# Kernel tuning notes

Hardware: AMD Instinct MI355X
Metric: run time of the kernel (lower is better)

Reference implementation:

```python
import jax, jax.numpy as jnp
import numpy as np

N = 100000
E = 1600000
IN_C, HID, OUT_C = 3, 64, 1


def setup_inputs() -> dict:
    key = jax.random.key(0)
    ks = jax.random.split(key, 12)
    x = jax.random.normal(ks[0], (N, IN_C), dtype=jnp.float32)
    edge_index = jax.random.randint(ks[1], (2, E), 0, N, dtype=jnp.int64)

    def glorot(k, shape):
        lim = np.sqrt(6.0 / (shape[0] + shape[1]))
        return jax.random.uniform(k, shape, jnp.float32, -lim, lim)

    return {
        "x": x,
        "edge_index": edge_index,
        "W1": glorot(ks[2], (IN_C, HID)), "b1": jnp.zeros((HID,), jnp.float32),
        "W2": glorot(ks[3], (HID, HID)), "b2": jnp.zeros((HID,), jnp.float32),
        "W3": glorot(ks[4], (HID, HID)), "b3": jnp.zeros((HID,), jnp.float32),
        "Wm1": glorot(ks[5], (HID, HID)), "bm1": jnp.zeros((HID,), jnp.float32),
        "Wm2": glorot(ks[6], (HID, OUT_C)), "bm2": jnp.zeros((OUT_C,), jnp.float32),
    }


def gcn_conv(x, src, dst, W, b):
    """PyG GCNConv: symmetric normalization with self-loops, linear, scatter-add, bias."""
    n = x.shape[0]
    loop = jnp.arange(n, dtype=src.dtype)
    s = jnp.concatenate([src, loop])
    d = jnp.concatenate([dst, loop])
    h = x @ W  # (N, out)
    deg = jax.ops.segment_sum(jnp.ones(s.shape[0], dtype=h.dtype), d, num_segments=n)
    dinv = jnp.where(deg > 0, 1.0 / jnp.sqrt(jnp.where(deg > 0, deg, 1.0)), 0.0)
    norm = dinv[s] * dinv[d]  # (E+N,)
    out = jax.ops.segment_sum(h[s] * norm[:, None], d, num_segments=n)
    return out + b


def reference(x, edge_index, W1, b1, W2, b2, W3, b3, Wm1, bm1, Wm2, bm2):
    src, dst = edge_index[0], edge_index[1]
    # 3 GCN layers with ReLU (dropout inactive in eval mode)
    h = jax.nn.relu(gcn_conv(x, src, dst, W1, b1))
    h = jax.nn.relu(gcn_conv(h, src, dst, W2, b2))
    h = jax.nn.relu(gcn_conv(h, src, dst, W3, b3))
    # MLP head + sigmoid
    h = jax.nn.relu(h @ Wm1 + bm1)
    out = jax.nn.sigmoid(h @ Wm2 + bm2)  # (N, 1)
    return out
```

## Files before the change

kernel.cpp:

```cpp
#include <hip/hip_runtime.h>
#include <hip/hip_fp16.h>
#include <math.h>

#define N_NODES 100000
#define N_EDGES 1600000
#define EP (N_EDGES + N_NODES)
#define HID 64
#define NCHUNK 250
#define CE (N_EDGES / NCHUNK)
#define NBUCK 782
#define CAP 2816
#define NTILE (N_NODES / 16)
#define STASH CAP
#define OBSTRIDE 512
#define NPN 4

typedef _Float16 half8_t __attribute__((ext_vector_type(8)));
typedef _Float16 half4_t __attribute__((ext_vector_type(4)));
typedef float f32x4_t __attribute__((ext_vector_type(4)));
typedef unsigned long long u64;



__global__ void init_kernel(int* __restrict__ gcur, int* __restrict__ csr) {
    int t = threadIdx.x;
    for (int b = t; b < NBUCK; b += 512) gcur[b] = b * CAP;
    if (t < 64) csr[EP + t] = 0;
}


__global__ __launch_bounds__(1024)
void scatter_kernel(const int* __restrict__ src, const int* __restrict__ dst,
                    int* __restrict__ gcur, unsigned* __restrict__ ebuf) {
    __shared__ int hist[NBUCK];
    __shared__ int cur[NBUCK];
    const int tid = threadIdx.x, c = blockIdx.x;
    for (int b = tid; b < NBUCK; b += 1024) hist[b] = 0;
    __syncthreads();
    const int4* d4p = (const int4*)(dst + c * CE);
    const int4* s4p = (const int4*)(src + c * CE);
    for (int t = tid; t < CE / 4; t += 1024) {
        int4 d = d4p[t];
        atomicAdd(&hist[d.x >> 7], 1);
        atomicAdd(&hist[d.y >> 7], 1);
        atomicAdd(&hist[d.z >> 7], 1);
        atomicAdd(&hist[d.w >> 7], 1);
    }
    __syncthreads();
    for (int b = tid; b < NBUCK; b += 1024)
        cur[b] = hist[b] ? atomicAdd(&gcur[b], hist[b]) : 0;
    __syncthreads();
    for (int t = tid; t < CE / 4; t += 1024) {
        int4 s = s4p[t];
        int4 d = d4p[t];
        int p0 = atomicAdd(&cur[d.x >> 7], 1);
        ebuf[p0] = ((unsigned)(d.x & 127) << 17) | (unsigned)s.x;
        int p1 = atomicAdd(&cur[d.y >> 7], 1);
        ebuf[p1] = ((unsigned)(d.y & 127) << 17) | (unsigned)s.y;
        int p2 = atomicAdd(&cur[d.z >> 7], 1);
        ebuf[p2] = ((unsigned)(d.z & 127) << 17) | (unsigned)s.z;
        int p3 = atomicAdd(&cur[d.w >> 7], 1);
        ebuf[p3] = ((unsigned)(d.w & 127) << 17) | (unsigned)s.w;
    }
}


__global__ void bscan_kernel(const int* __restrict__ gcur, int* __restrict__ bR0) {
    __shared__ int tmp[1024];
    int t = threadIdx.x;
    int v = (t < NBUCK) ? (gcur[t] - t * CAP + 128) : 0;
    tmp[t] = v;
    __syncthreads();
    for (int off = 1; off < 1024; off <<= 1) {
        int y = (t >= off) ? tmp[t - off] : 0;
        __syncthreads();
        tmp[t] += y;
        __syncthreads();
    }
    if (t < NBUCK) bR0[t] = tmp[t] - v;
}


__global__ __launch_bounds__(256)
void rankfill_kernel(const unsigned* __restrict__ ebuf, const int* __restrict__ gcur,
                     const int* __restrict__ bR0, u64* __restrict__ obuf,
                     int* __restrict__ rowptr, int* __restrict__ csr,
                     float* __restrict__ dinv,
                     const float* __restrict__ x, float4* __restrict__ xd) {
    __shared__ int cnt[128];
    __shared__ int rpl[128];
    __shared__ int wsum[2];
    __shared__ int ocnt;
    __shared__ unsigned stash[STASH];
    const int tid = threadIdx.x, b = blockIdx.x;
    if (tid < 128) cnt[tid] = 0;
    if (tid == 0) ocnt = 0;
    __syncthreads();
    const int E0 = b * CAP;
    const int RL = gcur[b] - E0;
    const int R0 = bR0[b];
    for (int off = tid; off < RL; off += 256) {
        unsigned v = ebuf[E0 + off];
        int key = (v >> 17) & 0x7F;
        int r = atomicAdd(&cnt[key], 1);
        if (r < 128) {
            stash[off] = ((unsigned)r << 24) | v;
        } else {
            stash[off] = 0xFFFFFFFFu;
            int oi = atomicAdd(&ocnt, 1);
            obuf[(size_t)b * OBSTRIDE + oi] =
                ((u64)r << 40) | ((u64)key << 32) | (u64)(v & 0x1FFFFu);
        }
    }
    __syncthreads();
    const int lane = tid & 63, w = tid >> 6;
    int xcnt = (tid < 128) ? cnt[tid] : 0;
    int inc = xcnt;
#pragma unroll
    for (int off = 1; off < 64; off <<= 1) {
        int y = __shfl_up(inc, off, 64);
        if (lane >= off) inc += y;
    }
    if (lane == 63 && w < 2) wsum[w] = inc;
    __syncthreads();
    if (tid < 128) {
        int base = (w == 1) ? wsum[0] : 0;
        int pre = base + inc - xcnt;
        const int n = b * 128 + tid;
        const int rpn = R0 + tid + pre;
        rpl[tid] = rpn;
        if (n < N_NODES) {
            rowptr[n] = rpn;
            float di = rsqrtf((float)(xcnt + 1));
            dinv[n] = di;
            csr[rpn + xcnt] = n;
            xd[n] = make_float4(x[n * 3 + 0] * di, x[n * 3 + 1] * di, x[n * 3 + 2] * di, 0.f);
        }
    }
    if (b == NBUCK - 1 && tid == 0) rowptr[N_NODES] = EP;
    __syncthreads();
    for (int off = tid; off < RL; off += 256) {
        unsigned v = stash[off];
        if (v == 0xFFFFFFFFu) continue;
        csr[rpl[(v >> 17) & 0x7F] + (v >> 24)] = (int)(v & 0x1FFFFu);
    }
    for (int j = tid; j < ocnt; j += 256) {
        u64 pk = obuf[(size_t)b * OBSTRIDE + j];
        csr[rpl[(pk >> 32) & 0xFF] + (int)(pk >> 40)] = (int)(pk & 0x1FFFFu);
    }
}


__device__ __forceinline__ void addp(float4& a, uint2 u, bool pred) {
    __half2 h0 = *(__half2*)&u.x, h1 = *(__half2*)&u.y;
    float2 x = __half22float2(h0), y = __half22float2(h1);
    if (pred) { a.x += x.x; a.y += x.y; a.z += y.x; a.w += y.y; }
}

__device__ __forceinline__ void bfly_store_lds(float4 acc, const float4 b4, float di,
                                               int g, int p, int l, _Float16* __restrict__ tl) {
    acc.x += __shfl_xor(acc.x, 16, 64);
    acc.y += __shfl_xor(acc.y, 16, 64);
    acc.z += __shfl_xor(acc.z, 16, 64);
    acc.w += __shfl_xor(acc.w, 16, 64);
    acc.x += __shfl_xor(acc.x, 32, 64);
    acc.y += __shfl_xor(acc.y, 32, 64);
    acc.z += __shfl_xor(acc.z, 32, 64);
    acc.w += __shfl_xor(acc.w, 32, 64);
    if (g == 0) {
        half4_t hv;
        hv[0] = (_Float16)fmaxf(fmaf(di, acc.x, b4.x), 0.f);
        hv[1] = (_Float16)fmaxf(fmaf(di, acc.y, b4.y), 0.f);
        hv[2] = (_Float16)fmaxf(fmaf(di, acc.z, b4.z), 0.f);
        hv[3] = (_Float16)fmaxf(fmaf(di, acc.w, b4.w), 0.f);
        *(half4_t*)(tl + l * 72 + p * 4) = hv;
    }
}

__device__ __forceinline__ void gather_phase(const __half* __restrict__ gf,
                                             const int* __restrict__ rowptr,
                                             const int* __restrict__ csr,
                                             const float* __restrict__ dinv,
                                             const float* __restrict__ bias,
                                             int n0, int lane, int wid,
                                             _Float16* __restrict__ tl) {
    const int g = lane >> 4, p = lane & 15;
    const int nw = n0 + wid * NPN;
    int rp = rowptr[nw + min(lane, NPN)];
    const uint2* gf2 = (const uint2*)gf;
    const float4 b4 = ((const float4*)bias)[p];
    int begv[NPN], cntv[NPN], idxv[NPN];
    int end_prev = __shfl(rp, 0, 64);
#pragma unroll
    for (int i = 0; i < NPN; ++i) {
        int end = __shfl(rp, i + 1, 64);
        begv[i] = end_prev;
        cntv[i] = end - end_prev;
        end_prev = end;
        idxv[i] = (lane < cntv[i]) ? csr[begv[i] + lane] : 0;
    }
#pragma unroll
    for (int ii = 0; ii < NPN; ii += 2) {
        const int la = wid * NPN + ii, lb = la + 1;
        const int ca = cntv[ii], cb = cntv[ii + 1];
        const int ba = begv[ii], bb = begv[ii + 1];
        const int iva = idxv[ii], ivb = idxv[ii + 1];
        int sa0 = __shfl(iva, g, 64),      sb0 = __shfl(ivb, g, 64);
        int sa1 = __shfl(iva, g + 4, 64),  sb1 = __shfl(ivb, g + 4, 64);
        int sa2 = __shfl(iva, g + 8, 64),  sb2 = __shfl(ivb, g + 8, 64);
        int sa3 = __shfl(iva, g + 12, 64), sb3 = __shfl(ivb, g + 12, 64);
        uint2 ua0 = gf2[(size_t)sa0 * 16 + p], ub0 = gf2[(size_t)sb0 * 16 + p];
        uint2 ua1 = gf2[(size_t)sa1 * 16 + p], ub1 = gf2[(size_t)sb1 * 16 + p];
        uint2 ua2 = gf2[(size_t)sa2 * 16 + p], ub2 = gf2[(size_t)sb2 * 16 + p];
        uint2 ua3 = gf2[(size_t)sa3 * 16 + p], ub3 = gf2[(size_t)sb3 * 16 + p];
        float4 accA = make_float4(0.f, 0.f, 0.f, 0.f);
        float4 accB = make_float4(0.f, 0.f, 0.f, 0.f);
        addp(accA, ua0, g + 0 < ca);  addp(accB, ub0, g + 0 < cb);
        addp(accA, ua1, g + 4 < ca);  addp(accB, ub1, g + 4 < cb);
        addp(accA, ua2, g + 8 < ca);  addp(accB, ub2, g + 8 < cb);
        addp(accA, ua3, g + 12 < ca); addp(accB, ub3, g + 12 < cb);
        if (ca > 16) {
#pragma unroll
            for (int k = 4; k < 8; ++k) {
                int e = g + 4 * k;
                int s = __shfl(iva, e, 64);
                addp(accA, gf2[(size_t)s * 16 + p], e < ca);
            }
            if (ca > 32) {
                for (int e = 32 + g; e < ca; e += 4) {
                    int s = (e < 64) ? __shfl(iva, e, 64) : csr[ba + e];
                    addp(accA, gf2[(size_t)s * 16 + p], true);
                }
            }
        }
        if (cb > 16) {
#pragma unroll
            for (int k = 4; k < 8; ++k) {
                int e = g + 4 * k;
                int s = __shfl(ivb, e, 64);
                addp(accB, gf2[(size_t)s * 16 + p], e < cb);
            }
            if (cb > 32) {
                for (int e = 32 + g; e < cb; e += 4) {
                    int s = (e < 64) ? __shfl(ivb, e, 64) : csr[bb + e];
                    addp(accB, gf2[(size_t)s * 16 + p], true);
                }
            }
        }
        bfly_store_lds(accA, b4, dinv[n0 + la], g, p, la, tl);
        bfly_store_lds(accB, b4, dinv[n0 + lb], g, p, lb, tl);
    }
}


__global__ __launch_bounds__(256, 8)
void fused_layer1_kernel(const float4* __restrict__ xd, const int* __restrict__ rowptr,
                         const int* __restrict__ csr, const float* __restrict__ dinv,
                         const float* __restrict__ b1, const float* __restrict__ W1,
                         const float* __restrict__ W2, __half* __restrict__ gf_out) {
    __shared__ __align__(16) _Float16 tile[16 * 72];
    __shared__ __align__(16) _Float16 tile2[16 * 72];
    const int tid = threadIdx.x;
    const int lane = tid & 63, wid = tid >> 6;
    const int n0 = blockIdx.x * 16;

    const int j = lane >> 4, p = lane & 15;
    const int l = wid * 4 + j;
    const int node = n0 + l;
    const int beg = rowptr[node], end = rowptr[node + 1];
    float a0 = 0.f, a1 = 0.f, a2 = 0.f;
    for (int e = beg + p; e < end; e += 16) {
        float4 v = xd[csr[e]];
        a0 += v.x; a1 += v.y; a2 += v.z;
    }
#pragma unroll
    for (int off = 1; off < 16; off <<= 1) {
        a0 += __shfl_xor(a0, off, 64);
        a1 += __shfl_xor(a1, off, 64);
        a2 += __shfl_xor(a2, off, 64);
    }
    const float dd = dinv[node];
    const float4 w0 = ((const float4*)W1)[p];
    const float4 w1 = ((const float4*)(W1 + HID))[p];
    const float4 w2 = ((const float4*)(W1 + 2 * HID))[p];
    const float4 bb = ((const float4*)b1)[p];
    half4_t hv;
    hv[0] = (_Float16)fmaxf(fmaf(dd, a0 * w0.x + a1 * w1.x + a2 * w2.x, bb.x), 0.f);
    hv[1] = (_Float16)fmaxf(fmaf(dd, a0 * w0.y + a1 * w1.y + a2 * w2.y, bb.y), 0.f);
    hv[2] = (_Float16)fmaxf(fmaf(dd, a0 * w0.z + a1 * w1.z + a2 * w2.z, bb.z), 0.f);
    hv[3] = (_Float16)fmaxf(fmaf(dd, a0 * w0.w + a1 * w1.w + a2 * w2.w, bb.w), 0.f);
    *(half4_t*)(tile + l * 72 + p * 4) = hv;
    __syncthreads();

    const int kg = lane >> 4, n = lane & 15;
    half8_t B0, B1;
#pragma unroll
    for (int jj = 0; jj < 8; ++jj) {
        B0[jj] = (_Float16)W2[(kg * 8 + jj) * HID + wid * 16 + n];
        B1[jj] = (_Float16)W2[(32 + kg * 8 + jj) * HID + wid * 16 + n];
    }
    half8_t A0 = *(const half8_t*)(tile + n * 72 + kg * 8);
    half8_t A1 = *(const half8_t*)(tile + n * 72 + 32 + kg * 8);
    f32x4_t c = {0.f, 0.f, 0.f, 0.f};
    c = __builtin_amdgcn_mfma_f32_16x16x32_f16(A0, B0, c, 0, 0, 0);
    c = __builtin_amdgcn_mfma_f32_16x16x32_f16(A1, B1, c, 0, 0, 0);

    const int q = lane >> 4;
#pragma unroll
    for (int r = 0; r < 4; ++r)
        tile2[(q * 4 + r) * 72 + wid * 16 + n] = (_Float16)(c[r] * dinv[n0 + q * 4 + r]);
    __syncthreads();
    const int row = tid >> 4, seg = tid & 15;
    uint2 v = *(const uint2*)(tile2 + row * 72 + seg * 4);
    *(uint2*)((__half*)gf_out + (size_t)(n0 + row) * HID + seg * 4) = v;
}

__global__ __launch_bounds__(256, 8)
void fused_layer_kernel(const __half* __restrict__ gf_in, const int* __restrict__ rowptr,
                        const int* __restrict__ csr, const float* __restrict__ dinv,
                        const float* __restrict__ bias, const float* __restrict__ W,
                        __half* __restrict__ gf_out) {
    __shared__ __align__(16) _Float16 tile[16 * 72];
    __shared__ __align__(16) _Float16 tile2[16 * 72];
    const int tid = threadIdx.x;
    const int lane = tid & 63, wid = tid >> 6;
    const int n0 = blockIdx.x * 16;

    gather_phase(gf_in, rowptr, csr, dinv, bias, n0, lane, wid, tile);
    __syncthreads();

    const int kg = lane >> 4, n = lane & 15;
    half8_t B0, B1;
#pragma unroll
    for (int j = 0; j < 8; ++j) {
        B0[j] = (_Float16)W[(kg * 8 + j) * HID + wid * 16 + n];
        B1[j] = (_Float16)W[(32 + kg * 8 + j) * HID + wid * 16 + n];
    }
    half8_t A0 = *(const half8_t*)(tile + n * 72 + kg * 8);
    half8_t A1 = *(const half8_t*)(tile + n * 72 + 32 + kg * 8);
    f32x4_t c = {0.f, 0.f, 0.f, 0.f};
    c = __builtin_amdgcn_mfma_f32_16x16x32_f16(A0, B0, c, 0, 0, 0);
    c = __builtin_amdgcn_mfma_f32_16x16x32_f16(A1, B1, c, 0, 0, 0);

    const int q = lane >> 4;
#pragma unroll
    for (int r = 0; r < 4; ++r)
        tile2[(q * 4 + r) * 72 + wid * 16 + n] = (_Float16)(c[r] * dinv[n0 + q * 4 + r]);
    __syncthreads();
    const int row = tid >> 4, seg = tid & 15;
    uint2 v = *(const uint2*)(tile2 + row * 72 + seg * 4);
    *(uint2*)((__half*)gf_out + (size_t)(n0 + row) * HID + seg * 4) = v;
}


__global__ __launch_bounds__(256, 8)
void fused_final_kernel(const __half* __restrict__ gf_in, const int* __restrict__ rowptr,
                        const int* __restrict__ csr, const float* __restrict__ dinv,
                        const float* __restrict__ b3, const float* __restrict__ Wm1,
                        const float* __restrict__ bm1, const float* __restrict__ Wm2,
                        const float* __restrict__ bm2, float* __restrict__ out) {
    __shared__ __align__(16) _Float16 tile[16 * 72];
    __shared__ float redbuf[4][16];
    const int tid = threadIdx.x;
    const int lane = tid & 63, wid = tid >> 6;
    const int n0 = blockIdx.x * 16;

    gather_phase(gf_in, rowptr, csr, dinv, b3, n0, lane, wid, tile);
    __syncthreads();

    const int kg = lane >> 4, n = lane & 15;
    half8_t B0, B1;
#pragma unroll
    for (int j = 0; j < 8; ++j) {
        B0[j] = (_Float16)Wm1[(kg * 8 + j) * HID + wid * 16 + n];
        B1[j] = (_Float16)Wm1[(32 + kg * 8 + j) * HID + wid * 16 + n];
    }
    half8_t A0 = *(const half8_t*)(tile + n * 72 + kg * 8);
    half8_t A1 = *(const half8_t*)(tile + n * 72 + 32 + kg * 8);
    f32x4_t c = {0.f, 0.f, 0.f, 0.f};
    c = __builtin_amdgcn_mfma_f32_16x16x32_f16(A0, B0, c, 0, 0, 0);
    c = __builtin_amdgcn_mfma_f32_16x16x32_f16(A1, B1, c, 0, 0, 0);

    const float bm1c = bm1[wid * 16 + n];
    const float wm2c = Wm2[wid * 16 + n];
    float part[4];
#pragma unroll
    for (int r = 0; r < 4; ++r) part[r] = fmaxf(c[r] + bm1c, 0.0f) * wm2c;
#pragma unroll
    for (int off = 1; off < 16; off <<= 1)
#pragma unroll
        for (int r = 0; r < 4; ++r) part[r] += __shfl_xor(part[r], off, 64);
    const int q = lane >> 4;
    if (n == 0) {
#pragma unroll
        for (int r = 0; r < 4; ++r) redbuf[wid][q * 4 + r] = part[r];
    }
    __syncthreads();
    if (tid < 16) {
        float s = redbuf[0][tid] + redbuf[1][tid] + redbuf[2][tid] + redbuf[3][tid];
        out[n0 + tid] = 1.0f / (1.0f + expf(-(s + bm2[0])));
    }
}


extern "C" void kernel_launch(void* const* d_in, const int* in_sizes, int n_in,
                              void* d_out, int out_size, void* d_ws, size_t ws_size,
                              hipStream_t stream) {
    const float* x   = (const float*)d_in[0];
    const int*   ei  = (const int*)d_in[1];
    const float* W1  = (const float*)d_in[2];
    const float* b1  = (const float*)d_in[3];
    const float* W2  = (const float*)d_in[4];
    const float* b2  = (const float*)d_in[5];
    const float* W3  = (const float*)d_in[6];
    const float* b3  = (const float*)d_in[7];
    const float* Wm1 = (const float*)d_in[8];
    const float* bm1 = (const float*)d_in[9];
    const float* Wm2 = (const float*)d_in[10];
    const float* bm2 = (const float*)d_in[11];
    float* out = (float*)d_out;

    const int* src = ei;
    const int* dst = ei + N_EDGES;

    char* ws = (char*)d_ws;
    size_t off = 0;
    auto alloc = [&](size_t bytes) { size_t o = off; off = (off + bytes + 255) & ~(size_t)255; return (void*)(ws + o); };
    int*      rowptr = (int*)alloc(4ll * (N_NODES + 1));
    int*      gcur   = (int*)alloc(4ll * NBUCK);
    int*      bR0    = (int*)alloc(4ll * NBUCK);
    int*      csr    = (int*)alloc(4ll * (EP + 64));
    float*    dinv   = (float*)alloc(4ll * N_NODES);
    float4*   xd     = (float4*)alloc(16ll * N_NODES);
    __half*   gfA    = (__half*)alloc(2ll * N_NODES * HID);
    __half*   gfB    = (__half*)alloc(2ll * N_NODES * HID);
    unsigned* ebuf   = (unsigned*)alloc(4ll * (size_t)NBUCK * CAP);
    u64*      obuf   = (u64*)alloc(8ll * (size_t)NBUCK * OBSTRIDE);
    (void)ws_size;

    init_kernel<<<1, 512, 0, stream>>>(gcur, csr);
    scatter_kernel<<<NCHUNK, 1024, 0, stream>>>(src, dst, gcur, ebuf);
    bscan_kernel<<<1, 1024, 0, stream>>>(gcur, bR0);
    rankfill_kernel<<<NBUCK, 256, 0, stream>>>(ebuf, gcur, bR0, obuf, rowptr, csr, dinv, x, xd);

    fused_layer1_kernel<<<NTILE, 256, 0, stream>>>(xd, rowptr, csr, dinv, b1, W1, W2, gfB);
    fused_layer_kernel<<<NTILE, 256, 0, stream>>>(gfB, rowptr, csr, dinv, b2, W3, gfA);
    fused_final_kernel<<<NTILE, 256, 0, stream>>>(gfA, rowptr, csr, dinv, b3, Wm1, bm1, Wm2, bm2, out);
}
```

Baseline: 207.6 us.

## Split feature gather into column-partitioned passes with separate transform kernels

Features are stored in four column-partitioned planes of 16 halves (32 bytes) per node. The gather runs as a separate kernel over blockIdx-major passes, so each pass touches only a quarter-sized working set that can stay resident in L2/MALL while neighbors are gathered at random. The MFMA transform and the MLP head then move into their own kernels that read the aggregated planes back. In exchange this adds two kernel launches and a full write and re-read of the aggregated features, and each gather pass reads the CSR again.

```diff
diff --git a/kernel.cpp b/kernel.cpp
--- a/kernel.cpp
+++ b/kernel.cpp
@@ -14,6 +14,8 @@
 #define STASH CAP
 #define OBSTRIDE 512
 #define NPN 4
+#define GT_NODES 32
+#define GT_TILES (N_NODES / GT_NODES)
 
 typedef _Float16 half8_t __attribute__((ext_vector_type(8)));
 typedef _Float16 half4_t __attribute__((ext_vector_type(4)));
@@ -21,13 +23,11 @@
 typedef unsigned long long u64;
 
 
-
 __global__ void init_kernel(int* __restrict__ gcur, int* __restrict__ csr) {
     int t = threadIdx.x;
     for (int b = t; b < NBUCK; b += 512) gcur[b] = b * CAP;
     if (t < 64) csr[EP + t] = 0;
 }
-
 
 __global__ __launch_bounds__(1024)
 void scatter_kernel(const int* __restrict__ src, const int* __restrict__ dst,
@@ -64,7 +64,6 @@
     }
 }
 
-
 __global__ void bscan_kernel(const int* __restrict__ gcur, int* __restrict__ bR0) {
     __shared__ int tmp[1024];
     int t = threadIdx.x;
@@ -79,7 +78,6 @@
     }
     if (t < NBUCK) bR0[t] = tmp[t] - v;
 }
-
 
 __global__ __launch_bounds__(256)
 void rankfill_kernel(const unsigned* __restrict__ ebuf, const int* __restrict__ gcur,
@@ -157,119 +155,184 @@
     if (pred) { a.x += x.x; a.y += x.y; a.z += y.x; a.w += y.y; }
 }
 
-__device__ __forceinline__ void bfly_store_lds(float4 acc, const float4 b4, float di,
-                                               int g, int p, int l, _Float16* __restrict__ tl) {
-    acc.x += __shfl_xor(acc.x, 16, 64);
-    acc.y += __shfl_xor(acc.y, 16, 64);
-    acc.z += __shfl_xor(acc.z, 16, 64);
-    acc.w += __shfl_xor(acc.w, 16, 64);
-    acc.x += __shfl_xor(acc.x, 32, 64);
-    acc.y += __shfl_xor(acc.y, 32, 64);
-    acc.z += __shfl_xor(acc.z, 32, 64);
-    acc.w += __shfl_xor(acc.w, 32, 64);
-    if (g == 0) {
-        half4_t hv;
-        hv[0] = (_Float16)fmaxf(fmaf(di, acc.x, b4.x), 0.f);
-        hv[1] = (_Float16)fmaxf(fmaf(di, acc.y, b4.y), 0.f);
-        hv[2] = (_Float16)fmaxf(fmaf(di, acc.z, b4.z), 0.f);
-        hv[3] = (_Float16)fmaxf(fmaf(di, acc.w, b4.w), 0.f);
-        *(half4_t*)(tl + l * 72 + p * 4) = hv;
-    }
-}
-
-__device__ __forceinline__ void gather_phase(const __half* __restrict__ gf,
-                                             const int* __restrict__ rowptr,
-                                             const int* __restrict__ csr,
-                                             const float* __restrict__ dinv,
-                                             const float* __restrict__ bias,
-                                             int n0, int lane, int wid,
-                                             _Float16* __restrict__ tl) {
-    const int g = lane >> 4, p = lane & 15;
-    const int nw = n0 + wid * NPN;
-    int rp = rowptr[nw + min(lane, NPN)];
-    const uint2* gf2 = (const uint2*)gf;
-    const float4 b4 = ((const float4*)bias)[p];
-    int begv[NPN], cntv[NPN], idxv[NPN];
-    int end_prev = __shfl(rp, 0, 64);
-#pragma unroll
-    for (int i = 0; i < NPN; ++i) {
-        int end = __shfl(rp, i + 1, 64);
-        begv[i] = end_prev;
-        cntv[i] = end - end_prev;
-        end_prev = end;
-        idxv[i] = (lane < cntv[i]) ? csr[begv[i] + lane] : 0;
-    }
-#pragma unroll
-    for (int ii = 0; ii < NPN; ii += 2) {
-        const int la = wid * NPN + ii, lb = la + 1;
-        const int ca = cntv[ii], cb = cntv[ii + 1];
-        const int ba = begv[ii], bb = begv[ii + 1];
-        const int iva = idxv[ii], ivb = idxv[ii + 1];
-        int sa0 = __shfl(iva, g, 64),      sb0 = __shfl(ivb, g, 64);
-        int sa1 = __shfl(iva, g + 4, 64),  sb1 = __shfl(ivb, g + 4, 64);
-        int sa2 = __shfl(iva, g + 8, 64),  sb2 = __shfl(ivb, g + 8, 64);
-        int sa3 = __shfl(iva, g + 12, 64), sb3 = __shfl(ivb, g + 12, 64);
-        uint2 ua0 = gf2[(size_t)sa0 * 16 + p], ub0 = gf2[(size_t)sb0 * 16 + p];
-        uint2 ua1 = gf2[(size_t)sa1 * 16 + p], ub1 = gf2[(size_t)sb1 * 16 + p];
-        uint2 ua2 = gf2[(size_t)sa2 * 16 + p], ub2 = gf2[(size_t)sb2 * 16 + p];
-        uint2 ua3 = gf2[(size_t)sa3 * 16 + p], ub3 = gf2[(size_t)sb3 * 16 + p];
+
+__global__ __launch_bounds__(256, 8)
+void gcol_kernel(const __half* __restrict__ gfc, const int* __restrict__ rowptr,
+                 const int* __restrict__ csr, const float* __restrict__ dinv,
+                 const float* __restrict__ bias, __half* __restrict__ agg) {
+    const int pass = blockIdx.x / GT_TILES;
+    const int tile = blockIdx.x % GT_TILES;
+    const int tid = threadIdx.x;
+    const int lane = tid & 63, wid = tid >> 6;
+    const int r = lane >> 2, c = lane & 3;
+    const uint2* g2 = (const uint2*)gfc + (size_t)pass * N_NODES * 4;
+    uint2* a2 = (uint2*)agg + (size_t)pass * N_NODES * 4;
+    const float4 bb = ((const float4*)bias)[pass * 4 + c];
+    const int nbase = tile * GT_NODES + wid * (GT_NODES / 4);
+#pragma unroll
+    for (int i = 0; i < GT_NODES / 4; i += 2) {
+        const int nA = nbase + i, nB = nbase + i + 1;
+        const int begA = rowptr[nA], endA = rowptr[nA + 1];
+        const int begB = rowptr[nB], endB = rowptr[nB + 1];
+        const int cA = endA - begA, cB = endB - begB;
+        int iA = (r < cA) ? csr[begA + r] : 0;
+        int iB = (r < cB) ? csr[begB + r] : 0;
+        uint2 uA = g2[(size_t)iA * 4 + c];
+        uint2 uB = g2[(size_t)iB * 4 + c];
         float4 accA = make_float4(0.f, 0.f, 0.f, 0.f);
         float4 accB = make_float4(0.f, 0.f, 0.f, 0.f);
-        addp(accA, ua0, g + 0 < ca);  addp(accB, ub0, g + 0 < cb);
-        addp(accA, ua1, g + 4 < ca);  addp(accB, ub1, g + 4 < cb);
-        addp(accA, ua2, g + 8 < ca);  addp(accB, ub2, g + 8 < cb);
-        addp(accA, ua3, g + 12 < ca); addp(accB, ub3, g + 12 < cb);
-        if (ca > 16) {
-#pragma unroll
-            for (int k = 4; k < 8; ++k) {
-                int e = g + 4 * k;
-                int s = __shfl(iva, e, 64);
-                addp(accA, gf2[(size_t)s * 16 + p], e < ca);
-            }
-            if (ca > 32) {
-                for (int e = 32 + g; e < ca; e += 4) {
-                    int s = (e < 64) ? __shfl(iva, e, 64) : csr[ba + e];
-                    addp(accA, gf2[(size_t)s * 16 + p], true);
-                }
-            }
-        }
-        if (cb > 16) {
-#pragma unroll
-            for (int k = 4; k < 8; ++k) {
-                int e = g + 4 * k;
-                int s = __shfl(ivb, e, 64);
-                addp(accB, gf2[(size_t)s * 16 + p], e < cb);
-            }
-            if (cb > 32) {
-                for (int e = 32 + g; e < cb; e += 4) {
-                    int s = (e < 64) ? __shfl(ivb, e, 64) : csr[bb + e];
-                    addp(accB, gf2[(size_t)s * 16 + p], true);
-                }
-            }
-        }
-        bfly_store_lds(accA, b4, dinv[n0 + la], g, p, la, tl);
-        bfly_store_lds(accB, b4, dinv[n0 + lb], g, p, lb, tl);
+        addp(accA, uA, r < cA);
+        addp(accB, uB, r < cB);
+        if (cA > 16) {
+            int r2 = 16 + r;
+            int i2 = (r2 < cA) ? csr[begA + r2] : 0;
+            addp(accA, g2[(size_t)i2 * 4 + c], r2 < cA);
+            for (int rr = 32 + r; rr < cA; rr += 16)
+                addp(accA, g2[(size_t)csr[begA + rr] * 4 + c], true);
+        }
+        if (cB > 16) {
+            int r2 = 16 + r;
+            int i2 = (r2 < cB) ? csr[begB + r2] : 0;
+            addp(accB, g2[(size_t)i2 * 4 + c], r2 < cB);
+            for (int rr = 32 + r; rr < cB; rr += 16)
+                addp(accB, g2[(size_t)csr[begB + rr] * 4 + c], true);
+        }
+#pragma unroll
+        for (int off = 4; off < 64; off <<= 1) {
+            accA.x += __shfl_xor(accA.x, off, 64);
+            accA.y += __shfl_xor(accA.y, off, 64);
+            accA.z += __shfl_xor(accA.z, off, 64);
+            accA.w += __shfl_xor(accA.w, off, 64);
+            accB.x += __shfl_xor(accB.x, off, 64);
+            accB.y += __shfl_xor(accB.y, off, 64);
+            accB.z += __shfl_xor(accB.z, off, 64);
+            accB.w += __shfl_xor(accB.w, off, 64);
+        }
+        if (r == 0) {
+            const float di = dinv[nA];
+            half4_t hv;
+            hv[0] = (_Float16)fmaxf(fmaf(di, accA.x, bb.x), 0.f);
+            hv[1] = (_Float16)fmaxf(fmaf(di, accA.y, bb.y), 0.f);
+            hv[2] = (_Float16)fmaxf(fmaf(di, accA.z, bb.z), 0.f);
+            hv[3] = (_Float16)fmaxf(fmaf(di, accA.w, bb.w), 0.f);
+            a2[(size_t)nA * 4 + c] = *(uint2*)&hv;
+        } else if (r == 1) {
+            const float di = dinv[nB];
+            half4_t hv;
+            hv[0] = (_Float16)fmaxf(fmaf(di, accB.x, bb.x), 0.f);
+            hv[1] = (_Float16)fmaxf(fmaf(di, accB.y, bb.y), 0.f);
+            hv[2] = (_Float16)fmaxf(fmaf(di, accB.z, bb.z), 0.f);
+            hv[3] = (_Float16)fmaxf(fmaf(di, accB.w, bb.w), 0.f);
+            a2[(size_t)nB * 4 + c] = *(uint2*)&hv;
+        }
     }
 }
 
 
 __global__ __launch_bounds__(256, 8)
-void fused_layer1_kernel(const float4* __restrict__ xd, const int* __restrict__ rowptr,
-                         const int* __restrict__ csr, const float* __restrict__ dinv,
-                         const float* __restrict__ b1, const float* __restrict__ W1,
-                         const float* __restrict__ W2, __half* __restrict__ gf_out) {
+void tcol_kernel(const __half* __restrict__ agg, const float* __restrict__ W,
+                 const float* __restrict__ dinv, __half* __restrict__ gfc_out) {
     __shared__ __align__(16) _Float16 tile[16 * 72];
     __shared__ __align__(16) _Float16 tile2[16 * 72];
     const int tid = threadIdx.x;
     const int lane = tid & 63, wid = tid >> 6;
     const int n0 = blockIdx.x * 16;
-
-    const int j = lane >> 4, p = lane & 15;
+    const int row = tid >> 4, seg = tid & 15;
+    const int p = seg >> 2, cc = seg & 3;
+    uint2 v = ((const uint2*)agg)[((size_t)p * N_NODES + n0 + row) * 4 + cc];
+    *(uint2*)(tile + row * 72 + seg * 4) = v;
+    __syncthreads();
+
+    const int kg = lane >> 4, n = lane & 15;
+    half8_t B0, B1;
+#pragma unroll
+    for (int j = 0; j < 8; ++j) {
+        B0[j] = (_Float16)W[(kg * 8 + j) * HID + wid * 16 + n];
+        B1[j] = (_Float16)W[(32 + kg * 8 + j) * HID + wid * 16 + n];
+    }
+    half8_t A0 = *(const half8_t*)(tile + n * 72 + kg * 8);
+    half8_t A1 = *(const half8_t*)(tile + n * 72 + 32 + kg * 8);
+    f32x4_t c = {0.f, 0.f, 0.f, 0.f};
+    c = __builtin_amdgcn_mfma_f32_16x16x32_f16(A0, B0, c, 0, 0, 0);
+    c = __builtin_amdgcn_mfma_f32_16x16x32_f16(A1, B1, c, 0, 0, 0);
+
+    const int q = lane >> 4;
+#pragma unroll
+    for (int rr = 0; rr < 4; ++rr)
+        tile2[(q * 4 + rr) * 72 + wid * 16 + n] = (_Float16)(c[rr] * dinv[n0 + q * 4 + rr]);
+    __syncthreads();
+    uint2 o = *(const uint2*)(tile2 + row * 72 + seg * 4);
+    ((uint2*)gfc_out)[((size_t)p * N_NODES + n0 + row) * 4 + cc] = o;
+}
+
+
+__global__ __launch_bounds__(256, 8)
+void tfinal_kernel(const __half* __restrict__ agg, const float* __restrict__ Wm1,
+                   const float* __restrict__ bm1, const float* __restrict__ Wm2,
+                   const float* __restrict__ bm2, float* __restrict__ out) {
+    __shared__ __align__(16) _Float16 tile[16 * 72];
+    __shared__ float redbuf[4][16];
+    const int tid = threadIdx.x;
+    const int lane = tid & 63, wid = tid >> 6;
+    const int n0 = blockIdx.x * 16;
+    const int row = tid >> 4, seg = tid & 15;
+    const int p = seg >> 2, cc = seg & 3;
+    uint2 v = ((const uint2*)agg)[((size_t)p * N_NODES + n0 + row) * 4 + cc];
+    *(uint2*)(tile + row * 72 + seg * 4) = v;
+    __syncthreads();
+
+    const int kg = lane >> 4, n = lane & 15;
+    half8_t B0, B1;
+#pragma unroll
+    for (int j = 0; j < 8; ++j) {
+        B0[j] = (_Float16)Wm1[(kg * 8 + j) * HID + wid * 16 + n];
+        B1[j] = (_Float16)Wm1[(32 + kg * 8 + j) * HID + wid * 16 + n];
+    }
+    half8_t A0 = *(const half8_t*)(tile + n * 72 + kg * 8);
+    half8_t A1 = *(const half8_t*)(tile + n * 72 + 32 + kg * 8);
+    f32x4_t c = {0.f, 0.f, 0.f, 0.f};
+    c = __builtin_amdgcn_mfma_f32_16x16x32_f16(A0, B0, c, 0, 0, 0);
+    c = __builtin_amdgcn_mfma_f32_16x16x32_f16(A1, B1, c, 0, 0, 0);
+
+    const float bm1c = bm1[wid * 16 + n];
+    const float wm2c = Wm2[wid * 16 + n];
+    float part[4];
+#pragma unroll
+    for (int r = 0; r < 4; ++r) part[r] = fmaxf(c[r] + bm1c, 0.0f) * wm2c;
+#pragma unroll
+    for (int off = 1; off < 16; off <<= 1)
+#pragma unroll
+        for (int r = 0; r < 4; ++r) part[r] += __shfl_xor(part[r], off, 64);
+    const int q = lane >> 4;
+    if (n == 0) {
+#pragma unroll
+        for (int r = 0; r < 4; ++r) redbuf[wid][q * 4 + r] = part[r];
+    }
+    __syncthreads();
+    if (tid < 16) {
+        float s = redbuf[0][tid] + redbuf[1][tid] + redbuf[2][tid] + redbuf[3][tid];
+        out[n0 + tid] = 1.0f / (1.0f + expf(-(s + bm2[0])));
+    }
+}
+
+
+__global__ __launch_bounds__(256, 8)
+void fused_layer1_kernel(const float4* __restrict__ xd, const int* __restrict__ rowptr,
+                         const int* __restrict__ csr, const float* __restrict__ dinv,
+                         const float* __restrict__ b1, const float* __restrict__ W1,
+                         const float* __restrict__ W2, __half* __restrict__ gfc_out) {
+    __shared__ __align__(16) _Float16 tile[16 * 72];
+    __shared__ __align__(16) _Float16 tile2[16 * 72];
+    const int tid = threadIdx.x;
+    const int lane = tid & 63, wid = tid >> 6;
+    const int n0 = blockIdx.x * 16;
+
+    const int j = lane >> 4, p0 = lane & 15;
     const int l = wid * 4 + j;
     const int node = n0 + l;
     const int beg = rowptr[node], end = rowptr[node + 1];
     float a0 = 0.f, a1 = 0.f, a2 = 0.f;
-    for (int e = beg + p; e < end; e += 16) {
+    for (int e = beg + p0; e < end; e += 16) {
         float4 v = xd[csr[e]];
         a0 += v.x; a1 += v.y; a2 += v.z;
     }
@@ -280,16 +343,16 @@
         a2 += __shfl_xor(a2, off, 64);
     }
     const float dd = dinv[node];
-    const float4 w0 = ((const float4*)W1)[p];
-    const float4 w1 = ((const float4*)(W1 + HID))[p];
-    const float4 w2 = ((const float4*)(W1 + 2 * HID))[p];
-    const float4 bb = ((const float4*)b1)[p];
+    const float4 w0 = ((const float4*)W1)[p0];
+    const float4 w1 = ((const float4*)(W1 + HID))[p0];
+    const float4 w2 = ((const float4*)(W1 + 2 * HID))[p0];
+    const float4 bb = ((const float4*)b1)[p0];
     half4_t hv;
     hv[0] = (_Float16)fmaxf(fmaf(dd, a0 * w0.x + a1 * w1.x + a2 * w2.x, bb.x), 0.f);
     hv[1] = (_Float16)fmaxf(fmaf(dd, a0 * w0.y + a1 * w1.y + a2 * w2.y, bb.y), 0.f);
     hv[2] = (_Float16)fmaxf(fmaf(dd, a0 * w0.z + a1 * w1.z + a2 * w2.z, bb.z), 0.f);
     hv[3] = (_Float16)fmaxf(fmaf(dd, a0 * w0.w + a1 * w1.w + a2 * w2.w, bb.w), 0.f);
-    *(half4_t*)(tile + l * 72 + p * 4) = hv;
+    *(half4_t*)(tile + l * 72 + p0 * 4) = hv;
     __syncthreads();
 
     const int kg = lane >> 4, n = lane & 15;
@@ -312,94 +375,7 @@
     __syncthreads();
     const int row = tid >> 4, seg = tid & 15;
     uint2 v = *(const uint2*)(tile2 + row * 72 + seg * 4);
-    *(uint2*)((__half*)gf_out + (size_t)(n0 + row) * HID + seg * 4) = v;
-}
-
-__global__ __launch_bounds__(256, 8)
-void fused_layer_kernel(const __half* __restrict__ gf_in, const int* __restrict__ rowptr,
-                        const int* __restrict__ csr, const float* __restrict__ dinv,
-                        const float* __restrict__ bias, const float* __restrict__ W,
-                        __half* __restrict__ gf_out) {
-    __shared__ __align__(16) _Float16 tile[16 * 72];
-    __shared__ __align__(16) _Float16 tile2[16 * 72];
-    const int tid = threadIdx.x;
-    const int lane = tid & 63, wid = tid >> 6;
-    const int n0 = blockIdx.x * 16;
-
-    gather_phase(gf_in, rowptr, csr, dinv, bias, n0, lane, wid, tile);
-    __syncthreads();
-
-    const int kg = lane >> 4, n = lane & 15;
-    half8_t B0, B1;
-#pragma unroll
-    for (int j = 0; j < 8; ++j) {
-        B0[j] = (_Float16)W[(kg * 8 + j) * HID + wid * 16 + n];
-        B1[j] = (_Float16)W[(32 + kg * 8 + j) * HID + wid * 16 + n];
-    }
-    half8_t A0 = *(const half8_t*)(tile + n * 72 + kg * 8);
-    half8_t A1 = *(const half8_t*)(tile + n * 72 + 32 + kg * 8);
-    f32x4_t c = {0.f, 0.f, 0.f, 0.f};
-    c = __builtin_amdgcn_mfma_f32_16x16x32_f16(A0, B0, c, 0, 0, 0);
-    c = __builtin_amdgcn_mfma_f32_16x16x32_f16(A1, B1, c, 0, 0, 0);
-
-    const int q = lane >> 4;
-#pragma unroll
-    for (int r = 0; r < 4; ++r)
-        tile2[(q * 4 + r) * 72 + wid * 16 + n] = (_Float16)(c[r] * dinv[n0 + q * 4 + r]);
-    __syncthreads();
-    const int row = tid >> 4, seg = tid & 15;
-    uint2 v = *(const uint2*)(tile2 + row * 72 + seg * 4);
-    *(uint2*)((__half*)gf_out + (size_t)(n0 + row) * HID + seg * 4) = v;
-}
-
-
-__global__ __launch_bounds__(256, 8)
-void fused_final_kernel(const __half* __restrict__ gf_in, const int* __restrict__ rowptr,
-                        const int* __restrict__ csr, const float* __restrict__ dinv,
-                        const float* __restrict__ b3, const float* __restrict__ Wm1,
-                        const float* __restrict__ bm1, const float* __restrict__ Wm2,
-                        const float* __restrict__ bm2, float* __restrict__ out) {
-    __shared__ __align__(16) _Float16 tile[16 * 72];
-    __shared__ float redbuf[4][16];
-    const int tid = threadIdx.x;
-    const int lane = tid & 63, wid = tid >> 6;
-    const int n0 = blockIdx.x * 16;
-
-    gather_phase(gf_in, rowptr, csr, dinv, b3, n0, lane, wid, tile);
-    __syncthreads();
-
-    const int kg = lane >> 4, n = lane & 15;
-    half8_t B0, B1;
-#pragma unroll
-    for (int j = 0; j < 8; ++j) {
-        B0[j] = (_Float16)Wm1[(kg * 8 + j) * HID + wid * 16 + n];
-        B1[j] = (_Float16)Wm1[(32 + kg * 8 + j) * HID + wid * 16 + n];
-    }
-    half8_t A0 = *(const half8_t*)(tile + n * 72 + kg * 8);
-    half8_t A1 = *(const half8_t*)(tile + n * 72 + 32 + kg * 8);
-    f32x4_t c = {0.f, 0.f, 0.f, 0.f};
-    c = __builtin_amdgcn_mfma_f32_16x16x32_f16(A0, B0, c, 0, 0, 0);
-    c = __builtin_amdgcn_mfma_f32_16x16x32_f16(A1, B1, c, 0, 0, 0);
-
-    const float bm1c = bm1[wid * 16 + n];
-    const float wm2c = Wm2[wid * 16 + n];
-    float part[4];
-#pragma unroll
-    for (int r = 0; r < 4; ++r) part[r] = fmaxf(c[r] + bm1c, 0.0f) * wm2c;
-#pragma unroll
-    for (int off = 1; off < 16; off <<= 1)
-#pragma unroll
-        for (int r = 0; r < 4; ++r) part[r] += __shfl_xor(part[r], off, 64);
-    const int q = lane >> 4;
-    if (n == 0) {
-#pragma unroll
-        for (int r = 0; r < 4; ++r) redbuf[wid][q * 4 + r] = part[r];
-    }
-    __syncthreads();
-    if (tid < 16) {
-        float s = redbuf[0][tid] + redbuf[1][tid] + redbuf[2][tid] + redbuf[3][tid];
-        out[n0 + tid] = 1.0f / (1.0f + expf(-(s + bm2[0])));
-    }
+    ((uint2*)gfc_out)[((size_t)(seg >> 2) * N_NODES + n0 + row) * 4 + (seg & 3)] = v;
 }
 
 
@@ -432,8 +408,10 @@
     int*      csr    = (int*)alloc(4ll * (EP + 64));
     float*    dinv   = (float*)alloc(4ll * N_NODES);
     float4*   xd     = (float4*)alloc(16ll * N_NODES);
-    __half*   gfA    = (__half*)alloc(2ll * N_NODES * HID);
-    __half*   gfB    = (__half*)alloc(2ll * N_NODES * HID);
+    __half*   gfc1   = (__half*)alloc(2ll * N_NODES * HID);
+    __half*   agg2   = (__half*)alloc(2ll * N_NODES * HID);
+    __half*   gfc2   = (__half*)alloc(2ll * N_NODES * HID);
+    __half*   aggF   = (__half*)alloc(2ll * N_NODES * HID);
     unsigned* ebuf   = (unsigned*)alloc(4ll * (size_t)NBUCK * CAP);
     u64*      obuf   = (u64*)alloc(8ll * (size_t)NBUCK * OBSTRIDE);
     (void)ws_size;
@@ -443,7 +421,11 @@
     bscan_kernel<<<1, 1024, 0, stream>>>(gcur, bR0);
     rankfill_kernel<<<NBUCK, 256, 0, stream>>>(ebuf, gcur, bR0, obuf, rowptr, csr, dinv, x, xd);
 
-    fused_layer1_kernel<<<NTILE, 256, 0, stream>>>(xd, rowptr, csr, dinv, b1, W1, W2, gfB);
-    fused_layer_kernel<<<NTILE, 256, 0, stream>>>(gfB, rowptr, csr, dinv, b2, W3, gfA);
-    fused_final_kernel<<<NTILE, 256, 0, stream>>>(gfA, rowptr, csr, dinv, b3, Wm1, bm1, Wm2, bm2, out);
-}
+    fused_layer1_kernel<<<NTILE, 256, 0, stream>>>(xd, rowptr, csr, dinv, b1, W1, W2, gfc1);
+
+    gcol_kernel<<<4 * GT_TILES, 256, 0, stream>>>(gfc1, rowptr, csr, dinv, b2, agg2);
+    tcol_kernel<<<NTILE, 256, 0, stream>>>(agg2, W3, dinv, gfc2);
+
+    gcol_kernel<<<4 * GT_TILES, 256, 0, stream>>>(gfc2, rowptr, csr, dinv, b3, aggF);
+    tfinal_kernel<<<NTILE, 256, 0, stream>>>(aggF, Wm1, bm1, Wm2, bm2, out);
+}
```

New measurement: 324.7 us. +56.4%, slower.

## Fold bucket scan into rankfill and stage CSR bucket in LDS

Applied to the files above, without the earlier changes.

Removes the separate single-block bucket prefix-scan launch; each rankfill block now computes its own base offset by summing the preceding bucket counts from global memory. The CSR segment for each bucket is assembled in shared memory through a second counting pass and then written to global memory with coalesced stores. This replaces the scattered global writes and the overflow buffer path. The cost is redundant per-block prefix work (up to 782 reads per block) and more LDS per block, which may reduce occupancy.

```diff
diff --git a/kernel.cpp b/kernel.cpp
--- a/kernel.cpp
+++ b/kernel.cpp
@@ -11,8 +11,6 @@
 #define NBUCK 782
 #define CAP 2816
 #define NTILE (N_NODES / 16)
-#define STASH CAP
-#define OBSTRIDE 512
 #define NPN 4
 
 typedef _Float16 half8_t __attribute__((ext_vector_type(8)));
@@ -21,13 +19,11 @@
 typedef unsigned long long u64;
 
 
-
 __global__ void init_kernel(int* __restrict__ gcur, int* __restrict__ csr) {
     int t = threadIdx.x;
     for (int b = t; b < NBUCK; b += 512) gcur[b] = b * CAP;
     if (t < 64) csr[EP + t] = 0;
 }
-
 
 __global__ __launch_bounds__(1024)
 void scatter_kernel(const int* __restrict__ src, const int* __restrict__ dst,
@@ -65,54 +61,37 @@
 }
 
 
-__global__ void bscan_kernel(const int* __restrict__ gcur, int* __restrict__ bR0) {
-    __shared__ int tmp[1024];
-    int t = threadIdx.x;
-    int v = (t < NBUCK) ? (gcur[t] - t * CAP + 128) : 0;
-    tmp[t] = v;
-    __syncthreads();
-    for (int off = 1; off < 1024; off <<= 1) {
-        int y = (t >= off) ? tmp[t - off] : 0;
-        __syncthreads();
-        tmp[t] += y;
-        __syncthreads();
-    }
-    if (t < NBUCK) bR0[t] = tmp[t] - v;
-}
-
-
 __global__ __launch_bounds__(256)
 void rankfill_kernel(const unsigned* __restrict__ ebuf, const int* __restrict__ gcur,
-                     const int* __restrict__ bR0, u64* __restrict__ obuf,
                      int* __restrict__ rowptr, int* __restrict__ csr,
                      float* __restrict__ dinv,
                      const float* __restrict__ x, float4* __restrict__ xd) {
+    __shared__ unsigned stash[CAP];
+    __shared__ int out[CAP + 128];
     __shared__ int cnt[128];
-    __shared__ int rpl[128];
+    __shared__ int cnt2[128];
+    __shared__ int rpl8[128];
     __shared__ int wsum[2];
-    __shared__ int ocnt;
-    __shared__ unsigned stash[STASH];
+    __shared__ int sR0;
     const int tid = threadIdx.x, b = blockIdx.x;
-    if (tid < 128) cnt[tid] = 0;
-    if (tid == 0) ocnt = 0;
-    __syncthreads();
+    if (tid < 128) { cnt[tid] = 0; cnt2[tid] = 0; }
+    if (tid == 0) sR0 = 0;
+    __syncthreads();
+
+    int acc = 0;
+    for (int i = tid; i < b; i += 256) acc += gcur[i] - i * CAP + 128;
+    if (acc) atomicAdd(&sR0, acc);
+
     const int E0 = b * CAP;
     const int RL = gcur[b] - E0;
-    const int R0 = bR0[b];
     for (int off = tid; off < RL; off += 256) {
         unsigned v = ebuf[E0 + off];
-        int key = (v >> 17) & 0x7F;
-        int r = atomicAdd(&cnt[key], 1);
-        if (r < 128) {
-            stash[off] = ((unsigned)r << 24) | v;
-        } else {
-            stash[off] = 0xFFFFFFFFu;
-            int oi = atomicAdd(&ocnt, 1);
-            obuf[(size_t)b * OBSTRIDE + oi] =
-                ((u64)r << 40) | ((u64)key << 32) | (u64)(v & 0x1FFFFu);
-        }
-    }
-    __syncthreads();
+        stash[off] = v;
+        atomicAdd(&cnt[(v >> 17) & 0x7F], 1);
+    }
+    __syncthreads();
+    const int R0 = sR0;
+
     const int lane = tid & 63, w = tid >> 6;
     int xcnt = (tid < 128) ? cnt[tid] : 0;
     int inc = xcnt;
@@ -125,29 +104,31 @@
     __syncthreads();
     if (tid < 128) {
         int base = (w == 1) ? wsum[0] : 0;
-        int pre = base + inc - xcnt;
+        int rel = tid + base + inc - xcnt;
+        rpl8[tid] = rel;
         const int n = b * 128 + tid;
-        const int rpn = R0 + tid + pre;
-        rpl[tid] = rpn;
         if (n < N_NODES) {
-            rowptr[n] = rpn;
+            rowptr[n] = R0 + rel;
             float di = rsqrtf((float)(xcnt + 1));
             dinv[n] = di;
-            csr[rpn + xcnt] = n;
+            out[rel + xcnt] = n;
             xd[n] = make_float4(x[n * 3 + 0] * di, x[n * 3 + 1] * di, x[n * 3 + 2] * di, 0.f);
         }
     }
     if (b == NBUCK - 1 && tid == 0) rowptr[N_NODES] = EP;
     __syncthreads();
+
     for (int off = tid; off < RL; off += 256) {
         unsigned v = stash[off];
-        if (v == 0xFFFFFFFFu) continue;
-        csr[rpl[(v >> 17) & 0x7F] + (v >> 24)] = (int)(v & 0x1FFFFu);
-    }
-    for (int j = tid; j < ocnt; j += 256) {
-        u64 pk = obuf[(size_t)b * OBSTRIDE + j];
-        csr[rpl[(pk >> 32) & 0xFF] + (int)(pk >> 40)] = (int)(pk & 0x1FFFFu);
-    }
+        int key = (v >> 17) & 0x7F;
+        int r = atomicAdd(&cnt2[key], 1);
+        out[rpl8[key] + r] = (int)(v & 0x1FFFFu);
+    }
+    __syncthreads();
+
+    const int nreal = min(128, N_NODES - b * 128);
+    const int lim = RL + nreal;
+    for (int i = tid; i < lim; i += 256) csr[R0 + i] = out[i];
 }
 
 
@@ -264,12 +245,12 @@
     const int lane = tid & 63, wid = tid >> 6;
     const int n0 = blockIdx.x * 16;
 
-    const int j = lane >> 4, p = lane & 15;
+    const int j = lane >> 4, p0 = lane & 15;
     const int l = wid * 4 + j;
     const int node = n0 + l;
     const int beg = rowptr[node], end = rowptr[node + 1];
     float a0 = 0.f, a1 = 0.f, a2 = 0.f;
-    for (int e = beg + p; e < end; e += 16) {
+    for (int e = beg + p0; e < end; e += 16) {
         float4 v = xd[csr[e]];
         a0 += v.x; a1 += v.y; a2 += v.z;
     }
@@ -280,16 +261,16 @@
         a2 += __shfl_xor(a2, off, 64);
     }
     const float dd = dinv[node];
-    const float4 w0 = ((const float4*)W1)[p];
-    const float4 w1 = ((const float4*)(W1 + HID))[p];
-    const float4 w2 = ((const float4*)(W1 + 2 * HID))[p];
-    const float4 bb = ((const float4*)b1)[p];
+    const float4 w0 = ((const float4*)W1)[p0];
+    const float4 w1 = ((const float4*)(W1 + HID))[p0];
+    const float4 w2 = ((const float4*)(W1 + 2 * HID))[p0];
+    const float4 bb = ((const float4*)b1)[p0];
     half4_t hv;
     hv[0] = (_Float16)fmaxf(fmaf(dd, a0 * w0.x + a1 * w1.x + a2 * w2.x, bb.x), 0.f);
     hv[1] = (_Float16)fmaxf(fmaf(dd, a0 * w0.y + a1 * w1.y + a2 * w2.y, bb.y), 0.f);
     hv[2] = (_Float16)fmaxf(fmaf(dd, a0 * w0.z + a1 * w1.z + a2 * w2.z, bb.z), 0.f);
     hv[3] = (_Float16)fmaxf(fmaf(dd, a0 * w0.w + a1 * w1.w + a2 * w2.w, bb.w), 0.f);
-    *(half4_t*)(tile + l * 72 + p * 4) = hv;
+    *(half4_t*)(tile + l * 72 + p0 * 4) = hv;
     __syncthreads();
 
     const int kg = lane >> 4, n = lane & 15;
@@ -428,20 +409,17 @@
     auto alloc = [&](size_t bytes) { size_t o = off; off = (off + bytes + 255) & ~(size_t)255; return (void*)(ws + o); };
     int*      rowptr = (int*)alloc(4ll * (N_NODES + 1));
     int*      gcur   = (int*)alloc(4ll * NBUCK);
-    int*      bR0    = (int*)alloc(4ll * NBUCK);
     int*      csr    = (int*)alloc(4ll * (EP + 64));
     float*    dinv   = (float*)alloc(4ll * N_NODES);
     float4*   xd     = (float4*)alloc(16ll * N_NODES);
     __half*   gfA    = (__half*)alloc(2ll * N_NODES * HID);
     __half*   gfB    = (__half*)alloc(2ll * N_NODES * HID);
     unsigned* ebuf   = (unsigned*)alloc(4ll * (size_t)NBUCK * CAP);
-    u64*      obuf   = (u64*)alloc(8ll * (size_t)NBUCK * OBSTRIDE);
     (void)ws_size;
 
     init_kernel<<<1, 512, 0, stream>>>(gcur, csr);
     scatter_kernel<<<NCHUNK, 1024, 0, stream>>>(src, dst, gcur, ebuf);
-    bscan_kernel<<<1, 1024, 0, stream>>>(gcur, bR0);
-    rankfill_kernel<<<NBUCK, 256, 0, stream>>>(ebuf, gcur, bR0, obuf, rowptr, csr, dinv, x, xd);
+    rankfill_kernel<<<NBUCK, 256, 0, stream>>>(ebuf, gcur, rowptr, csr, dinv, x, xd);
 
     fused_layer1_kernel<<<NTILE, 256, 0, stream>>>(xd, rowptr, csr, dinv, b1, W1, W2, gfB);
     fused_layer_kernel<<<NTILE, 256, 0, stream>>>(gfB, rowptr, csr, dinv, b2, W3, gfA);
```

After: 202.4 us. 2.5% less time.
